# Kernel tuning notes

Hardware: AMD Instinct MI355X
Metric: run time of the kernel (lower is better)

Reference implementation:

```python
import jax, jax.numpy as jnp
import numpy as np

N = 100000   # nodes
E = 1000000  # directed edges (before self-loops)
G = 512      # graphs in the batch
NEG_SLOPE = 0.2
EPS = 1e-5


def setup_inputs() -> dict:
    key = jax.random.key(0)
    ks = jax.random.split(key, 24)
    r = lambda i, shape, s=0.1: (jax.random.normal(ks[i], shape) * s).astype(jnp.float32)
    return {
        'x': jax.random.normal(ks[0], (N, 27), dtype=jnp.float32),
        'edge_index': jax.random.randint(ks[1], (2, E), 0, N, dtype=jnp.int32),
        'batch': jnp.sort(jax.random.randint(ks[2], (N,), 0, G, dtype=jnp.int32)),
        # GATv2Conv(26, 32, heads=2)
        'Wl1': r(3, (26, 64)), 'bl1': jnp.zeros(64, jnp.float32),
        'Wr1': r(4, (26, 64)), 'br1': jnp.zeros(64, jnp.float32),
        'att1': r(5, (2, 32)), 'b1': jnp.zeros(64, jnp.float32),
        'g1': jnp.ones(64, jnp.float32), 'be1': jnp.zeros(64, jnp.float32),
        # GATv2Conv(64, 32, heads=1)
        'Wl2': r(6, (64, 32)), 'bl2': jnp.zeros(32, jnp.float32),
        'Wr2': r(7, (64, 32)), 'br2': jnp.zeros(32, jnp.float32),
        'att2': r(8, (1, 32)), 'b2': jnp.zeros(32, jnp.float32),
        'g2': jnp.ones(32, jnp.float32), 'be2': jnp.zeros(32, jnp.float32),
        # gate_nn: 32 -> 16 -> 1
        'Wg1': r(9, (32, 16)), 'bg1': jnp.zeros(16, jnp.float32),
        'Wg2': r(10, (16, 1)), 'bg2': jnp.zeros(1, jnp.float32),
        # final head: 33 -> 16 -> 1
        'Wh1': r(11, (33, 16)), 'bh1': jnp.zeros(16, jnp.float32),
        'Wh2': r(12, (16, 1)), 'bh2': jnp.zeros(1, jnp.float32),
    }


def _gatv2(x, Wl, bl, Wr, br, att, bias, src, dst, heads, ch):
    n = x.shape[0]
    xl = (x @ Wl + bl).reshape(n, heads, ch)  # source projection (messages)
    xr = (x @ Wr + br).reshape(n, heads, ch)  # target projection
    e = jax.nn.leaky_relu(xl[src] + xr[dst], NEG_SLOPE)      # [Etot, H, C]
    logits = jnp.einsum('ehc,hc->eh', e, att)                 # [Etot, H]
    m = jax.ops.segment_max(logits, dst, num_segments=n)
    a = jnp.exp(logits - m[dst])
    z = jax.ops.segment_sum(a, dst, num_segments=n)
    a = a / (z[dst] + 1e-16)
    out = jax.ops.segment_sum(xl[src] * a[:, :, None], dst, num_segments=n)
    return out.reshape(n, heads * ch) + bias


def _batchnorm(h, gamma, beta):
    mu = h.mean(axis=0)
    var = jnp.var(h, axis=0)  # biased, matches torch normalization
    return (h - mu) * jax.lax.rsqrt(var + EPS) * gamma + beta


def reference(x, edge_index, batch, Wl1, bl1, Wr1, br1, att1, b1, g1, be1,
              Wl2, bl2, Wr2, br2, att2, b2, g2, be2,
              Wg1, bg1, Wg2, bg2, Wh1, bh1, Wh2, bh2):
    n = x.shape[0]
    loops = jnp.arange(n, dtype=edge_index.dtype)
    src = jnp.concatenate([edge_index[0], loops])
    dst = jnp.concatenate([edge_index[1], loops])
    x_no_cost = jnp.concatenate([x[:, :24], x[:, 25:]], axis=1)  # [N, 26]
    h = jax.nn.elu(_batchnorm(_gatv2(x_no_cost, Wl1, bl1, Wr1, br1, att1, b1, src, dst, 2, 32), g1, be1))
    # dropout is identity in eval mode
    h = jax.nn.elu(_batchnorm(_gatv2(h, Wl2, bl2, Wr2, br2, att2, b2, src, dst, 1, 32), g2, be2))
    # attentional aggregation: gate MLP + segment softmax over graphs
    gate = jax.nn.relu(h @ Wg1 + bg1) @ Wg2 + bg2               # [N, 1]
    gm = jax.ops.segment_max(gate, batch, num_segments=G)
    ga = jnp.exp(gate - gm[batch])
    gz = jax.ops.segment_sum(ga, batch, num_segments=G)
    ga = ga / (gz[batch] + 1e-16)
    h_pooled = jax.ops.segment_sum(ga * h, batch, num_segments=G)  # [G, 32]
    counts = jax.ops.segment_sum(jnp.ones((n, 1), x.dtype), batch, num_segments=G)
    root_costs = jax.ops.segment_sum(x[:, 24:25], batch, num_segments=G) / jnp.maximum(counts, 1.0)
    combined = jnp.concatenate([h_pooled, root_costs], axis=1)   # [G, 33]
    return jax.nn.relu(combined @ Wh1 + bh1) @ Wh2 + bh2         # [G, 1]
```

## Files before the change

### kernel.cpp

```cpp
#include <hip/hip_runtime.h>
#include <hip/hip_fp16.h>
#include <math.h>

#define NEG 0.2f
#define BN_EPS 1e-5f
#define BKT_W 256
#define CHUNK 4096


__global__ __launch_bounds__(256)
void hist_kernel(const int* __restrict__ ei, int E, int nbh, int nbkt, int* __restrict__ cnt)
{
    __shared__ int hist[512];
    for (int i = threadIdx.x; i < nbkt; i += 256) hist[i] = 0;
    __syncthreads();
    const int g0 = blockIdx.x * (CHUNK / 4);
    #pragma unroll
    for (int it = 0; it < CHUNK / 1024; ++it) {
        int e = (g0 + it * 256 + threadIdx.x) * 4;
        if (e + 3 < E) {
            int4 d4 = *(const int4*)(ei + E + e);
            atomicAdd(&hist[d4.x >> 8], 1);
            atomicAdd(&hist[d4.y >> 8], 1);
            atomicAdd(&hist[d4.z >> 8], 1);
            atomicAdd(&hist[d4.w >> 8], 1);
        } else {
            for (int k = 0; k < 4; ++k)
                if (e + k < E) atomicAdd(&hist[ei[E + e + k] >> 8], 1);
        }
    }
    __syncthreads();
    for (int i = threadIdx.x; i < nbkt; i += 256) cnt[(size_t)i * nbh + blockIdx.x] = hist[i];
}

__global__ __launch_bounds__(256)
void scan_block_kernel(const int* __restrict__ in, int* __restrict__ out,
                       int* __restrict__ bsum, int n)
{
    __shared__ int s[256];
    int i = blockIdx.x * 256 + threadIdx.x;
    int v = (i < n) ? in[i] : 0;
    s[threadIdx.x] = v;
    __syncthreads();
    for (int off = 1; off < 256; off <<= 1) {
        int t = (threadIdx.x >= off) ? s[threadIdx.x - off] : 0;
        __syncthreads();
        s[threadIdx.x] += t;
        __syncthreads();
    }
    if (i < n) out[i + 1] = s[threadIdx.x];
    if (threadIdx.x == 255) bsum[blockIdx.x] = s[255];
}

__global__ __launch_bounds__(512)
void scan_sums_kernel(int* __restrict__ bsum, int nb)
{
    __shared__ int s[512];
    int v = (threadIdx.x < nb) ? bsum[threadIdx.x] : 0;
    s[threadIdx.x] = v;
    __syncthreads();
    for (int off = 1; off < 512; off <<= 1) {
        int t = (threadIdx.x >= off) ? s[threadIdx.x - off] : 0;
        __syncthreads();
        s[threadIdx.x] += t;
        __syncthreads();
    }
    if (threadIdx.x < nb) bsum[threadIdx.x] = s[threadIdx.x] - v;
}

__global__ __launch_bounds__(256)
void scan_add_kernel(int* __restrict__ out, const int* __restrict__ bsum, int n)
{
    int i = blockIdx.x * 256 + threadIdx.x;
    if (i < n) out[i + 1] += bsum[blockIdx.x];
    if (i == 0) out[0] = 0;
}

__global__ __launch_bounds__(256)
void scat_kernel(const int* __restrict__ ei, int E, int nbh, int nbkt,
                 const int* __restrict__ base, int2* __restrict__ pairs)
{
    __shared__ int fill[512];
    __shared__ int lbase[512];
    for (int i = threadIdx.x; i < nbkt; i += 256) {
        fill[i]  = 0;
        lbase[i] = base[(size_t)i * nbh + blockIdx.x];
    }
    __syncthreads();
    const int g0 = blockIdx.x * (CHUNK / 4);
    #pragma unroll
    for (int it = 0; it < CHUNK / 1024; ++it) {
        int e = (g0 + it * 256 + threadIdx.x) * 4;
        if (e + 3 < E) {
            int4 s4 = *(const int4*)(ei + e);
            int4 d4 = *(const int4*)(ei + E + e);
            int b, r;
            b = d4.x >> 8; r = atomicAdd(&fill[b], 1); pairs[lbase[b] + r] = make_int2(s4.x, d4.x);
            b = d4.y >> 8; r = atomicAdd(&fill[b], 1); pairs[lbase[b] + r] = make_int2(s4.y, d4.y);
            b = d4.z >> 8; r = atomicAdd(&fill[b], 1); pairs[lbase[b] + r] = make_int2(s4.z, d4.z);
            b = d4.w >> 8; r = atomicAdd(&fill[b], 1); pairs[lbase[b] + r] = make_int2(s4.w, d4.w);
        } else {
            for (int k = 0; k < 4; ++k) {
                if (e + k < E) {
                    int s = ei[e + k], d = ei[E + e + k];
                    int b = d >> 8;
                    int r = atomicAdd(&fill[b], 1);
                    pairs[lbase[b] + r] = make_int2(s, d);
                }
            }
        }
    }
}

__global__ __launch_bounds__(256)
void bucket_build_kernel(const int2* __restrict__ pairs, const int* __restrict__ base,
                         int nbh, int nbkt, int n, int E,
                         int* __restrict__ rowptr, int* __restrict__ srcs,
                         int* __restrict__ perm)
{
    const int b     = blockIdx.x;
    const int start = base[(size_t)b * nbh];
    const int end   = base[(size_t)(b + 1) * nbh];
    __shared__ int hist[256], sc[256], dcnt[64], dbase[64];
    hist[threadIdx.x] = 0;
    if (threadIdx.x < 64) dcnt[threadIdx.x] = 0;
    __syncthreads();
    for (int j = start + threadIdx.x; j < end; j += 256)
        atomicAdd(&hist[pairs[j].y & 255], 1);
    __syncthreads();
    const int v = hist[threadIdx.x];
    sc[threadIdx.x] = v;
    __syncthreads();
    for (int off = 1; off < 256; off <<= 1) {
        int t = (threadIdx.x >= off) ? sc[threadIdx.x - off] : 0;
        __syncthreads();
        sc[threadIdx.x] += t;
        __syncthreads();
    }
    const int excl = sc[threadIdx.x] - v;
    const int d = b * 256 + threadIdx.x;
    int bin = 0, rnk = 0;
    if (d < n) {
        rowptr[d] = start + excl;
        bin = min(v, 63);
        rnk = atomicAdd(&dcnt[bin], 1);
    }
    if (b == nbkt - 1 && threadIdx.x == 0) rowptr[n] = E;
    __syncthreads();
    hist[threadIdx.x] = excl;
    __syncthreads();
    for (int j = start + threadIdx.x; j < end; j += 256) {
        int2 p = pairs[j];
        int r = atomicAdd(&hist[p.y & 255], 1);
        srcs[start + r] = p.x;
    }
    if (threadIdx.x < 64) dbase[threadIdx.x] = dcnt[threadIdx.x];
    __syncthreads();
    for (int off = 1; off < 64; off <<= 1) {
        int t = 0;
        if (threadIdx.x < 64 && threadIdx.x >= off) t = dbase[threadIdx.x - off];
        __syncthreads();
        if (threadIdx.x < 64) dbase[threadIdx.x] += t;
        __syncthreads();
    }
    if (d < n) perm[b * 256 + (dbase[bin] - dcnt[bin]) + rnk] = d;
}


__device__ __forceinline__ void gat_step4(const uint2 raw, const float* __restrict__ xrv,
                                          const float* __restrict__ at,
                                          float& z, float* __restrict__ acc)
{
    union { uint2 u; __half2 h[2]; } q; q.u = raw;
    const float2 a = __half22float2(q.h[0]);
    const float2 b = __half22float2(q.h[1]);
    float t, p = 0.f;
    t = a.x + xrv[0]; t = t > 0.f ? t : NEG * t; p += t * at[0];
    t = a.y + xrv[1]; t = t > 0.f ? t : NEG * t; p += t * at[1];
    t = b.x + xrv[2]; t = t > 0.f ? t : NEG * t; p += t * at[2];
    t = b.y + xrv[3]; t = t > 0.f ? t : NEG * t; p += t * at[3];
    p += __shfl_xor(p, 1, 64);
    p += __shfl_xor(p, 2, 64);
    p += __shfl_xor(p, 4, 64);
    const float w = __expf(p);
    z += w;
    acc[0] += w * a.x; acc[1] += w * a.y; acc[2] += w * b.x; acc[3] += w * b.y;
}

template<int HC>
__global__ __launch_bounds__(256)
void gat_fused_kernel(const __half* __restrict__ xl, const float* __restrict__ xr,
                      const float* __restrict__ att,
                      const int* __restrict__ rowptr, const int* __restrict__ srcs,
                      const int* __restrict__ perm,
                      float* __restrict__ outp, int n)
{
    constexpr int LPG = HC / 4;
    const int gid  = (blockIdx.x * 256 + threadIdx.x) / LPG;
    const int lane = threadIdx.x % LPG;
    if (gid >= n) return;
    const int d = perm[gid];

    float at[4], xrv[4];
    {
        const float4 a = *(const float4*)(att + lane * 4);
        at[0] = a.x; at[1] = a.y; at[2] = a.z; at[3] = a.w;
        const float4 x0 = *(const float4*)(xr + (size_t)d * HC + lane * 4);
        xrv[0] = x0.x; xrv[1] = x0.y; xrv[2] = x0.z; xrv[3] = x0.w;
    }

    float z = 0.f, acc[4] = {0.f, 0.f, 0.f, 0.f};
    gat_step4(*(const uint2*)(xl + (size_t)d * HC + lane * 4), xrv, at, z, acc);

    const int jb = rowptr[d], je = rowptr[d + 1];
    int j = jb;
    for (; j + 4 <= je; j += 4) {
        const int s0 = srcs[j], s1 = srcs[j + 1], s2 = srcs[j + 2], s3 = srcs[j + 3];
        const uint2 r0 = *(const uint2*)(xl + (size_t)s0 * HC + lane * 4);
        const uint2 r1 = *(const uint2*)(xl + (size_t)s1 * HC + lane * 4);
        const uint2 r2 = *(const uint2*)(xl + (size_t)s2 * HC + lane * 4);
        const uint2 r3 = *(const uint2*)(xl + (size_t)s3 * HC + lane * 4);
        gat_step4(r0, xrv, at, z, acc);
        gat_step4(r1, xrv, at, z, acc);
        gat_step4(r2, xrv, at, z, acc);
        gat_step4(r3, xrv, at, z, acc);
    }
    for (; j < je; ++j)
        gat_step4(*(const uint2*)(xl + (size_t)srcs[j] * HC + lane * 4), xrv, at, z, acc);

    const float inv = 1.f / (z + 1e-16f);
    *(float4*)(outp + (size_t)d * HC + lane * 4) =
        make_float4(acc[0] * inv, acc[1] * inv, acc[2] * inv, acc[3] * inv);
}

template<int K, int OC, bool DROP24, bool FUSE_NORM>
__global__ __launch_bounds__(256, 4)
void proj_kernel(const float* __restrict__ in, int in_stride,
                 const float* __restrict__ Wl, const float* __restrict__ bl,
                 const float* __restrict__ Wr, const float* __restrict__ br,
                 const float* __restrict__ stats, const float* __restrict__ gamma,
                 const float* __restrict__ beta, float inv_n,
                 __half* __restrict__ outl, float* __restrict__ outr, int n)
{
    constexpr int C2  = 2 * OC;
    constexpr int NCG = C2 / 4;
    constexpr int NRG = 256 / NCG;
    constexpr int TR  = NRG * 4;
    constexpr int XLD = (K + 3) & ~3;
    __shared__ float xs[TR][XLD];

    float na = 1.f, nb = 0.f;
    if constexpr (FUSE_NORM) {
        int kk  = threadIdx.x % K;
        float mu  = stats[kk] * inv_n;
        float var = stats[K + kk] * inv_n - mu * mu;
        float rs  = rsqrtf(var + BN_EPS) * gamma[kk];
        na = rs; nb = beta[kk] - mu * rs;
    }

    const int row0 = blockIdx.x * TR;
    for (int i = threadIdx.x; i < TR * K; i += 256) {
        int r = i / K, k = i - r * K;
        int row = row0 + r;
        float v = 0.f;
        if (row < n) {
            int sc = DROP24 ? (k < 24 ? k : k + 1) : k;
            v = in[(size_t)row * in_stride + sc];
            if constexpr (FUSE_NORM) {
                float t = v * na + nb;
                v = t > 0.f ? t : expm1f(t);
            }
        }
        xs[r][k] = v;
    }
    __syncthreads();

    const int cg = threadIdx.x % NCG;
    const int rg = threadIdx.x / NCG;
    const int c4 = cg * 4;
    const bool left = (c4 < OC);
    const float* __restrict__ Wp = left ? Wl : Wr;
    const int cc = left ? c4 : c4 - OC;
    const float4 b4 = *(const float4*)((left ? bl : br) + cc);

    float acc[4][4];
    #pragma unroll
    for (int ri = 0; ri < 4; ++ri) {
        acc[ri][0] = b4.x; acc[ri][1] = b4.y; acc[ri][2] = b4.z; acc[ri][3] = b4.w;
    }

    #pragma unroll 1
    for (int kb = 0; kb < K / 4; ++kb) {
        const float4 w0 = *(const float4*)(Wp + (size_t)(kb * 4 + 0) * OC + cc);
        const float4 w1 = *(const float4*)(Wp + (size_t)(kb * 4 + 1) * OC + cc);
        const float4 w2 = *(const float4*)(Wp + (size_t)(kb * 4 + 2) * OC + cc);
        const float4 w3 = *(const float4*)(Wp + (size_t)(kb * 4 + 3) * OC + cc);
        #pragma unroll
        for (int ri = 0; ri < 4; ++ri) {
            const float4 xv = *(const float4*)(&xs[rg * 4 + ri][kb * 4]);
            acc[ri][0] += xv.x * w0.x + xv.y * w1.x + xv.z * w2.x + xv.w * w3.x;
            acc[ri][1] += xv.x * w0.y + xv.y * w1.y + xv.z * w2.y + xv.w * w3.y;
            acc[ri][2] += xv.x * w0.z + xv.y * w1.z + xv.z * w2.z + xv.w * w3.z;
            acc[ri][3] += xv.x * w0.w + xv.y * w1.w + xv.z * w2.w + xv.w * w3.w;
        }
    }
    if constexpr ((K & 3) != 0) {
        #pragma unroll
        for (int k = K & ~3; k < K; ++k) {
            const float4 wk = *(const float4*)(Wp + (size_t)k * OC + cc);
            #pragma unroll
            for (int ri = 0; ri < 4; ++ri) {
                const float xk = xs[rg * 4 + ri][k];
                acc[ri][0] += xk * wk.x; acc[ri][1] += xk * wk.y;
                acc[ri][2] += xk * wk.z; acc[ri][3] += xk * wk.w;
            }
        }
    }

    #pragma unroll
    for (int ri = 0; ri < 4; ++ri) {
        const int row = row0 + rg * 4 + ri;
        if (row >= n) continue;
        if (left) {
            union { uint2 u; __half2 h[2]; } o;
            o.h[0] = __float22half2_rn(make_float2(acc[ri][0], acc[ri][1]));
            o.h[1] = __float22half2_rn(make_float2(acc[ri][2], acc[ri][3]));
            *(uint2*)(outl + (size_t)row * OC + cc) = o.u;
        } else {
            *(float4*)(outr + (size_t)row * OC + cc) =
                make_float4(acc[ri][0], acc[ri][1], acc[ri][2], acc[ri][3]);
        }
    }
}

template<int C>
__global__ __launch_bounds__(256)
void bn_stats_kernel(const float* __restrict__ h, int n, float* __restrict__ stats)
{
    constexpr int RPB = 256 / C;
    int col = threadIdx.x % C, rg = threadIdx.x / C;
    float s = 0.f, s2 = 0.f;
    for (int r = blockIdx.x * RPB + rg; r < n; r += gridDim.x * RPB) {
        float v = h[(size_t)r * C + col];
        s += v; s2 += v * v;
    }
    __shared__ float red0[256], red1[256];
    red0[threadIdx.x] = s; red1[threadIdx.x] = s2;
    __syncthreads();
    for (int st = 128; st >= C; st >>= 1) {
        if (threadIdx.x < st) {
            red0[threadIdx.x] += red0[threadIdx.x + st];
            red1[threadIdx.x] += red1[threadIdx.x + st];
        }
        __syncthreads();
    }
    if (threadIdx.x < C) {
        atomicAdd(&stats[threadIdx.x],     red0[threadIdx.x]);
        atomicAdd(&stats[C + threadIdx.x], red1[threadIdx.x]);
    }
}

__global__ __launch_bounds__(256)
void gate_norm_kernel(float* __restrict__ h2, int n,
                      const float* __restrict__ stats, const float* __restrict__ gamma,
                      const float* __restrict__ beta, float inv_n,
                      const float* __restrict__ Wg1, const float* __restrict__ bg1,
                      const float* __restrict__ Wg2, const float* __restrict__ bg2,
                      float* __restrict__ gate)
{
    __shared__ float W1[512], W2[16], B1[16], A_[32], B_[32];
    for (int i = threadIdx.x; i < 512; i += 256) W1[i] = Wg1[i];
    if (threadIdx.x < 16) { W2[threadIdx.x] = Wg2[threadIdx.x]; B1[threadIdx.x] = bg1[threadIdx.x]; }
    if (threadIdx.x < 32) {
        float mu  = stats[threadIdx.x] * inv_n;
        float var = stats[32 + threadIdx.x] * inv_n - mu * mu;
        float rs  = rsqrtf(var + BN_EPS) * gamma[threadIdx.x];
        A_[threadIdx.x] = rs;
        B_[threadIdx.x] = beta[threadIdx.x] - mu * rs;
    }
    __syncthreads();
    int node = blockIdx.x * 256 + threadIdx.x;
    if (node >= n) return;
    float* row = h2 + (size_t)node * 32;
    float v[32];
    #pragma unroll
    for (int j = 0; j < 8; ++j) {
        float4 r = *(const float4*)(row + j * 4);
        v[4*j] = r.x; v[4*j+1] = r.y; v[4*j+2] = r.z; v[4*j+3] = r.w;
    }
    #pragma unroll
    for (int k = 0; k < 32; ++k) {
        float t = v[k] * A_[k] + B_[k];
        v[k] = t > 0.f ? t : expm1f(t);
    }
    float hid[16];
    #pragma unroll
    for (int j = 0; j < 16; ++j) hid[j] = B1[j];
    #pragma unroll
    for (int k = 0; k < 32; ++k) {
        #pragma unroll
        for (int j = 0; j < 16; ++j) hid[j] += v[k] * W1[k * 16 + j];
    }
    float g = bg2[0];
    #pragma unroll
    for (int j = 0; j < 16; ++j) g += (hid[j] > 0.f ? hid[j] : 0.f) * W2[j];
    gate[node] = g;
    #pragma unroll
    for (int j = 0; j < 8; ++j)
        *(float4*)(row + j * 4) = make_float4(v[4*j], v[4*j+1], v[4*j+2], v[4*j+3]);
}

__global__ __launch_bounds__(256)
void pool_head_kernel(const float* __restrict__ h2, const float* __restrict__ gate,
                      const int* __restrict__ batch, const float* __restrict__ x,
                      int n, int xstride,
                      const float* __restrict__ Wh1, const float* __restrict__ bh1,
                      const float* __restrict__ Wh2, const float* __restrict__ bh2,
                      float* __restrict__ out)
{
    int g = blockIdx.x;
    __shared__ int sstart, send;
    if (threadIdx.x == 0) {
        int lo = 0, hi = n;
        while (lo < hi) { int mid = (lo + hi) >> 1; if (batch[mid] < g) lo = mid + 1; else hi = mid; }
        sstart = lo;
        hi = n;
        while (lo < hi) { int mid = (lo + hi) >> 1; if (batch[mid] < g + 1) lo = mid + 1; else hi = mid; }
        send = lo;
    }
    __syncthreads();
    const int start = sstart, end = send, cnt = end - start;

    __shared__ float red[256];
    float mx = -INFINITY;
    for (int i = start + threadIdx.x; i < end; i += 256) mx = fmaxf(mx, gate[i]);
    red[threadIdx.x] = mx; __syncthreads();
    for (int st = 128; st > 0; st >>= 1) {
        if (threadIdx.x < st) red[threadIdx.x] = fmaxf(red[threadIdx.x], red[threadIdx.x + st]);
        __syncthreads();
    }
    const float gm = red[0]; __syncthreads();

    float se = 0.f;
    for (int i = start + threadIdx.x; i < end; i += 256) se += expf(gate[i] - gm);
    red[threadIdx.x] = se; __syncthreads();
    for (int st = 128; st > 0; st >>= 1) {
        if (threadIdx.x < st) red[threadIdx.x] += red[threadIdx.x + st];
        __syncthreads();
    }
    const float gz = red[0]; __syncthreads();

    float rc = 0.f;
    for (int i = start + threadIdx.x; i < end; i += 256) rc += x[(size_t)i * xstride + 24];
    red[threadIdx.x] = rc; __syncthreads();
    for (int st = 128; st > 0; st >>= 1) {
        if (threadIdx.x < st) red[threadIdx.x] += red[threadIdx.x + st];
        __syncthreads();
    }
    const float root = red[0] / fmaxf((float)cnt, 1.f); __syncthreads();

    const int col = threadIdx.x % 32, rg = threadIdx.x / 32;
    float acc = 0.f;
    for (int i = start + rg; i < end; i += 8) acc += expf(gate[i] - gm) * h2[(size_t)i * 32 + col];
    red[threadIdx.x] = acc; __syncthreads();
    for (int st = 128; st >= 32; st >>= 1) {
        if (threadIdx.x < st) red[threadIdx.x] += red[threadIdx.x + st];
        __syncthreads();
    }
    __shared__ float comb[33];
    if (threadIdx.x < 32) comb[threadIdx.x] = red[threadIdx.x] / (gz + 1e-16f);
    if (threadIdx.x == 0) comb[32] = root;
    __syncthreads();

    __shared__ float hidr[16];
    if (threadIdx.x < 16) {
        float hv = bh1[threadIdx.x];
        #pragma unroll
        for (int k = 0; k < 33; ++k) hv += comb[k] * Wh1[k * 16 + threadIdx.x];
        hidr[threadIdx.x] = hv > 0.f ? hv : 0.f;
    }
    __syncthreads();
    if (threadIdx.x == 0) {
        float r = bh2[0];
        #pragma unroll
        for (int j = 0; j < 16; ++j) r += hidr[j] * Wh2[j];
        out[g] = r;
    }
}


extern "C" void kernel_launch(void* const* d_in, const int* in_sizes, int n_in,
                              void* d_out, int out_size, void* d_ws, size_t ws_size,
                              hipStream_t stream)
{
    const float* x    = (const float*)d_in[0];
    const int*   ei   = (const int*)d_in[1];
    const int*   batch= (const int*)d_in[2];
    const float* Wl1  = (const float*)d_in[3];
    const float* bl1  = (const float*)d_in[4];
    const float* Wr1  = (const float*)d_in[5];
    const float* br1  = (const float*)d_in[6];
    const float* att1 = (const float*)d_in[7];
    const float* g1   = (const float*)d_in[9];
    const float* be1  = (const float*)d_in[10];
    const float* Wl2  = (const float*)d_in[11];
    const float* bl2  = (const float*)d_in[12];
    const float* Wr2  = (const float*)d_in[13];
    const float* br2  = (const float*)d_in[14];
    const float* att2 = (const float*)d_in[15];
    const float* g2   = (const float*)d_in[17];
    const float* be2  = (const float*)d_in[18];
    const float* Wg1  = (const float*)d_in[19];
    const float* bg1  = (const float*)d_in[20];
    const float* Wg2  = (const float*)d_in[21];
    const float* bg2  = (const float*)d_in[22];
    const float* Wh1  = (const float*)d_in[23];
    const float* bh1  = (const float*)d_in[24];
    const float* Wh2  = (const float*)d_in[25];
    const float* bh2  = (const float*)d_in[26];

    const int n  = in_sizes[0] / 27;
    const int E  = in_sizes[1] / 2;
    const int G  = out_size;
    const float inv_n = 1.f / (float)n;

    const int nbkt = (n + BKT_W - 1) / BKT_W;
    const int nbh  = (E + CHUNK - 1) / CHUNK;
    const int SZ   = nbkt * nbh;
    const int NBs  = (SZ + 255) / 256;

    float* ws = (float*)d_ws;
    size_t off = 0;
    auto align4 = [&](size_t v) { return (v + 3) & ~(size_t)3; };
    float* st1 = ws + off; off += 128;
    float* st2 = ws + off; off += 64;
    const size_t zero_floats = off;
    int* cnt     = (int*)(ws + off); off = align4(off + SZ);
    int* basearr = (int*)(ws + off); off = align4(off + SZ + 1);
    int* bsum    = (int*)(ws + off); off = align4(off + 512);
    int* rowptr  = (int*)(ws + off); off = align4(off + n + 1);
    int* srcs    = (int*)(ws + off); off = align4(off + E);
    int* perm    = (int*)(ws + off); off = align4(off + n);
    __half* xl1h = (__half*)(ws + off); off += (size_t)n * 32;
    float* xr1   = ws + off; off += (size_t)n * 64;
    float* h1    = ws + off; off += (size_t)n * 64;
    float* h2    = ws + off; off += (size_t)n * 32;
    int2* pairs   = (int2*)h1;
    __half* xl2h  = xl1h;
    float* xr2    = xr1;
    float* gate   = xr1 + (size_t)n * 32;

    hipMemsetAsync(d_ws, 0, zero_floats * sizeof(float), stream);

    hist_kernel<<<nbh, 256, 0, stream>>>(ei, E, nbh, nbkt, cnt);
    scan_block_kernel<<<NBs, 256, 0, stream>>>(cnt, basearr, bsum, SZ);
    scan_sums_kernel<<<1, 512, 0, stream>>>(bsum, NBs);
    scan_add_kernel<<<NBs, 256, 0, stream>>>(basearr, bsum, SZ);
    scat_kernel<<<nbh, 256, 0, stream>>>(ei, E, nbh, nbkt, basearr, pairs);
    bucket_build_kernel<<<nbkt, 256, 0, stream>>>(pairs, basearr, nbh, nbkt, n, E, rowptr, srcs, perm);

    proj_kernel<26, 64, true, false><<<(n + 31) / 32, 256, 0, stream>>>(
        x, 27, Wl1, bl1, Wr1, br1, nullptr, nullptr, nullptr, 0.f, xl1h, xr1, n);
    gat_fused_kernel<64><<<(n * 16 + 255) / 256, 256, 0, stream>>>(
        xl1h, xr1, att1, rowptr, srcs, perm, h1, n);
    bn_stats_kernel<64><<<256, 256, 0, stream>>>(h1, n, st1);

    proj_kernel<64, 32, false, true><<<(n + 63) / 64, 256, 0, stream>>>(
        h1, 64, Wl2, bl2, Wr2, br2, st1, g1, be1, inv_n, xl2h, xr2, n);
    gat_fused_kernel<32><<<(n * 8 + 255) / 256, 256, 0, stream>>>(
        xl2h, xr2, att2, rowptr, srcs, perm, h2, n);
    bn_stats_kernel<32><<<256, 256, 0, stream>>>(h2, n, st2);

    gate_norm_kernel<<<(n + 255) / 256, 256, 0, stream>>>(
        h2, n, st2, g2, be2, inv_n, Wg1, bg1, Wg2, bg2, gate);
    pool_head_kernel<<<G, 256, 0, stream>>>(h2, gate, batch, x, n, 27, Wh1, bh1, Wh2, bh2, (float*)d_out);
}
```

Measured before the change: 263.0 us.

## Fuse layer-1 projection into histogram kernel and store intermediates in half

The layer-1 projection now runs as extra blocks of the edge histogram kernel, so both overlap in one launch. The target projections xr and the layer-1 GAT output h1 are stored in fp16 instead of fp32, which halves their memory traffic in the GAT, BN-stats and layer-2 projection kernels. The BN-stats grid is enlarged to 1024 blocks. The cost is lower precision for h1 and the xr values, plus a heterogeneous fused kernel.

```diff
diff --git a/kernel.cpp b/kernel.cpp
--- a/kernel.cpp
+++ b/kernel.cpp
@@ -8,29 +8,102 @@
 #define CHUNK 4096
 
 
-__global__ __launch_bounds__(256)
-void hist_kernel(const int* __restrict__ ei, int E, int nbh, int nbkt, int* __restrict__ cnt)
+__global__ __launch_bounds__(256, 4)
+void hist_proj1_kernel(const int* __restrict__ ei, int E, int nbh, int nbkt,
+                       int* __restrict__ cnt,
+                       const float* __restrict__ in, int in_stride,
+                       const float* __restrict__ Wl, const float* __restrict__ bl,
+                       const float* __restrict__ Wr, const float* __restrict__ br,
+                       __half* __restrict__ outl, __half* __restrict__ outr, int n)
 {
     __shared__ int hist[512];
-    for (int i = threadIdx.x; i < nbkt; i += 256) hist[i] = 0;
-    __syncthreads();
-    const int g0 = blockIdx.x * (CHUNK / 4);
-    #pragma unroll
-    for (int it = 0; it < CHUNK / 1024; ++it) {
-        int e = (g0 + it * 256 + threadIdx.x) * 4;
-        if (e + 3 < E) {
-            int4 d4 = *(const int4*)(ei + E + e);
-            atomicAdd(&hist[d4.x >> 8], 1);
-            atomicAdd(&hist[d4.y >> 8], 1);
-            atomicAdd(&hist[d4.z >> 8], 1);
-            atomicAdd(&hist[d4.w >> 8], 1);
-        } else {
-            for (int k = 0; k < 4; ++k)
-                if (e + k < E) atomicAdd(&hist[ei[E + e + k] >> 8], 1);
-        }
-    }
-    __syncthreads();
-    for (int i = threadIdx.x; i < nbkt; i += 256) cnt[(size_t)i * nbh + blockIdx.x] = hist[i];
+    __shared__ float xs[32][28];
+
+    if (blockIdx.x < nbh) {
+        const int bid = blockIdx.x;
+        for (int i = threadIdx.x; i < nbkt; i += 256) hist[i] = 0;
+        __syncthreads();
+        const int g0 = bid * (CHUNK / 4);
+        #pragma unroll
+        for (int it = 0; it < CHUNK / 1024; ++it) {
+            int e = (g0 + it * 256 + threadIdx.x) * 4;
+            if (e + 3 < E) {
+                int4 d4 = *(const int4*)(ei + E + e);
+                atomicAdd(&hist[d4.x >> 8], 1);
+                atomicAdd(&hist[d4.y >> 8], 1);
+                atomicAdd(&hist[d4.z >> 8], 1);
+                atomicAdd(&hist[d4.w >> 8], 1);
+            } else {
+                for (int k = 0; k < 4; ++k)
+                    if (e + k < E) atomicAdd(&hist[ei[E + e + k] >> 8], 1);
+            }
+        }
+        __syncthreads();
+        for (int i = threadIdx.x; i < nbkt; i += 256) cnt[(size_t)i * nbh + bid] = hist[i];
+    } else {
+        constexpr int K = 26, OC = 64, NCG = 32;
+        const int row0 = (blockIdx.x - nbh) * 32;
+        for (int i = threadIdx.x; i < 32 * K; i += 256) {
+            int r = i / K, k = i - r * K;
+            int row = row0 + r;
+            float v = 0.f;
+            if (row < n) {
+                int sc = (k < 24) ? k : k + 1;
+                v = in[(size_t)row * in_stride + sc];
+            }
+            xs[r][k] = v;
+        }
+        __syncthreads();
+
+        const int cg = threadIdx.x % NCG;
+        const int rg = threadIdx.x / NCG;
+        const int c4 = cg * 4;
+        const bool left = (c4 < OC);
+        const float* __restrict__ Wp = left ? Wl : Wr;
+        const int cc = left ? c4 : c4 - OC;
+        const float4 b4 = *(const float4*)((left ? bl : br) + cc);
+
+        float acc[4][4];
+        #pragma unroll
+        for (int ri = 0; ri < 4; ++ri) {
+            acc[ri][0] = b4.x; acc[ri][1] = b4.y; acc[ri][2] = b4.z; acc[ri][3] = b4.w;
+        }
+        #pragma unroll 1
+        for (int kb = 0; kb < K / 4; ++kb) {
+            const float4 w0 = *(const float4*)(Wp + (size_t)(kb * 4 + 0) * OC + cc);
+            const float4 w1 = *(const float4*)(Wp + (size_t)(kb * 4 + 1) * OC + cc);
+            const float4 w2 = *(const float4*)(Wp + (size_t)(kb * 4 + 2) * OC + cc);
+            const float4 w3 = *(const float4*)(Wp + (size_t)(kb * 4 + 3) * OC + cc);
+            #pragma unroll
+            for (int ri = 0; ri < 4; ++ri) {
+                const float4 xv = *(const float4*)(&xs[rg * 4 + ri][kb * 4]);
+                acc[ri][0] += xv.x * w0.x + xv.y * w1.x + xv.z * w2.x + xv.w * w3.x;
+                acc[ri][1] += xv.x * w0.y + xv.y * w1.y + xv.z * w2.y + xv.w * w3.y;
+                acc[ri][2] += xv.x * w0.z + xv.y * w1.z + xv.z * w2.z + xv.w * w3.z;
+                acc[ri][3] += xv.x * w0.w + xv.y * w1.w + xv.z * w2.w + xv.w * w3.w;
+            }
+        }
+        #pragma unroll
+        for (int k = 24; k < K; ++k) {
+            const float4 wk = *(const float4*)(Wp + (size_t)k * OC + cc);
+            #pragma unroll
+            for (int ri = 0; ri < 4; ++ri) {
+                const float xk = xs[rg * 4 + ri][k];
+                acc[ri][0] += xk * wk.x; acc[ri][1] += xk * wk.y;
+                acc[ri][2] += xk * wk.z; acc[ri][3] += xk * wk.w;
+            }
+        }
+        __half* __restrict__ outp = left ? outl : outr;
+        #pragma unroll
+        for (int ri = 0; ri < 4; ++ri) {
+            const int row = row0 + rg * 4 + ri;
+            if (row >= n) continue;
+            union { uint2 u; __half2 h[2]; } o;
+            o.h[0] = __float22half2_rn(make_float2(acc[ri][0], acc[ri][1]));
+            o.h[1] = __float22half2_rn(make_float2(acc[ri][2], acc[ri][3]));
+            *(uint2*)(outp + (size_t)row * OC + cc) = o.u;
+        }
+    }
 }
 
 __global__ __launch_bounds__(256)
@@ -187,13 +260,13 @@
     acc[0] += w * a.x; acc[1] += w * a.y; acc[2] += w * b.x; acc[3] += w * b.y;
 }
 
-template<int HC>
-__global__ __launch_bounds__(256)
-void gat_fused_kernel(const __half* __restrict__ xl, const float* __restrict__ xr,
+template<int HC, bool OUT_HALF>
+__global__ __launch_bounds__(256)
+void gat_fused_kernel(const __half* __restrict__ xl, const __half* __restrict__ xr,
                       const float* __restrict__ att,
                       const int* __restrict__ rowptr, const int* __restrict__ srcs,
                       const int* __restrict__ perm,
-                      float* __restrict__ outp, int n)
+                      void* __restrict__ outp, int n)
 {
     constexpr int LPG = HC / 4;
     const int gid  = (blockIdx.x * 256 + threadIdx.x) / LPG;
@@ -205,8 +278,11 @@
     {
         const float4 a = *(const float4*)(att + lane * 4);
         at[0] = a.x; at[1] = a.y; at[2] = a.z; at[3] = a.w;
-        const float4 x0 = *(const float4*)(xr + (size_t)d * HC + lane * 4);
-        xrv[0] = x0.x; xrv[1] = x0.y; xrv[2] = x0.z; xrv[3] = x0.w;
+        union { uint2 u; __half2 h[2]; } qx;
+        qx.u = *(const uint2*)(xr + (size_t)d * HC + lane * 4);
+        const float2 x0 = __half22float2(qx.h[0]);
+        const float2 x1 = __half22float2(qx.h[1]);
+        xrv[0] = x0.x; xrv[1] = x0.y; xrv[2] = x1.x; xrv[3] = x1.y;
     }
 
     float z = 0.f, acc[4] = {0.f, 0.f, 0.f, 0.f};
@@ -229,34 +305,37 @@
         gat_step4(*(const uint2*)(xl + (size_t)srcs[j] * HC + lane * 4), xrv, at, z, acc);
 
     const float inv = 1.f / (z + 1e-16f);
-    *(float4*)(outp + (size_t)d * HC + lane * 4) =
-        make_float4(acc[0] * inv, acc[1] * inv, acc[2] * inv, acc[3] * inv);
-}
-
-template<int K, int OC, bool DROP24, bool FUSE_NORM>
+    if constexpr (OUT_HALF) {
+        union { uint2 u; __half2 h[2]; } o;
+        o.h[0] = __float22half2_rn(make_float2(acc[0] * inv, acc[1] * inv));
+        o.h[1] = __float22half2_rn(make_float2(acc[2] * inv, acc[3] * inv));
+        *(uint2*)((__half*)outp + (size_t)d * HC + lane * 4) = o.u;
+    } else {
+        *(float4*)((float*)outp + (size_t)d * HC + lane * 4) =
+            make_float4(acc[0] * inv, acc[1] * inv, acc[2] * inv, acc[3] * inv);
+    }
+}
+
+template<int K, int OC>
 __global__ __launch_bounds__(256, 4)
-void proj_kernel(const float* __restrict__ in, int in_stride,
-                 const float* __restrict__ Wl, const float* __restrict__ bl,
-                 const float* __restrict__ Wr, const float* __restrict__ br,
-                 const float* __restrict__ stats, const float* __restrict__ gamma,
-                 const float* __restrict__ beta, float inv_n,
-                 __half* __restrict__ outl, float* __restrict__ outr, int n)
+void proj2_kernel(const __half* __restrict__ in,
+                  const float* __restrict__ Wl, const float* __restrict__ bl,
+                  const float* __restrict__ Wr, const float* __restrict__ br,
+                  const float* __restrict__ stats, const float* __restrict__ gamma,
+                  const float* __restrict__ beta, float inv_n,
+                  __half* __restrict__ outl, __half* __restrict__ outr, int n)
 {
     constexpr int C2  = 2 * OC;
     constexpr int NCG = C2 / 4;
     constexpr int NRG = 256 / NCG;
     constexpr int TR  = NRG * 4;
-    constexpr int XLD = (K + 3) & ~3;
-    __shared__ float xs[TR][XLD];
-
-    float na = 1.f, nb = 0.f;
-    if constexpr (FUSE_NORM) {
-        int kk  = threadIdx.x % K;
-        float mu  = stats[kk] * inv_n;
-        float var = stats[K + kk] * inv_n - mu * mu;
-        float rs  = rsqrtf(var + BN_EPS) * gamma[kk];
-        na = rs; nb = beta[kk] - mu * rs;
-    }
+    __shared__ float xs[TR][K];
+
+    const int kk  = threadIdx.x % K;
+    const float mu  = stats[kk] * inv_n;
+    const float var = stats[K + kk] * inv_n - mu * mu;
+    const float rs  = rsqrtf(var + BN_EPS) * gamma[kk];
+    const float na = rs, nb = beta[kk] - mu * rs;
 
     const int row0 = blockIdx.x * TR;
     for (int i = threadIdx.x; i < TR * K; i += 256) {
@@ -264,12 +343,8 @@
         int row = row0 + r;
         float v = 0.f;
         if (row < n) {
-            int sc = DROP24 ? (k < 24 ? k : k + 1) : k;
-            v = in[(size_t)row * in_stride + sc];
-            if constexpr (FUSE_NORM) {
-                float t = v * na + nb;
-                v = t > 0.f ? t : expm1f(t);
-            }
+            float t = __half2float(in[(size_t)row * K + k]) * na + nb;
+            v = t > 0.f ? t : expm1f(t);
         }
         xs[r][k] = v;
     }
@@ -304,44 +379,30 @@
             acc[ri][3] += xv.x * w0.w + xv.y * w1.w + xv.z * w2.w + xv.w * w3.w;
         }
     }
-    if constexpr ((K & 3) != 0) {
-        #pragma unroll
-        for (int k = K & ~3; k < K; ++k) {
-            const float4 wk = *(const float4*)(Wp + (size_t)k * OC + cc);
-            #pragma unroll
-            for (int ri = 0; ri < 4; ++ri) {
-                const float xk = xs[rg * 4 + ri][k];
-                acc[ri][0] += xk * wk.x; acc[ri][1] += xk * wk.y;
-                acc[ri][2] += xk * wk.z; acc[ri][3] += xk * wk.w;
-            }
-        }
-    }
-
+
+    __half* __restrict__ outp = left ? outl : outr;
     #pragma unroll
     for (int ri = 0; ri < 4; ++ri) {
         const int row = row0 + rg * 4 + ri;
         if (row >= n) continue;
-        if (left) {
-            union { uint2 u; __half2 h[2]; } o;
-            o.h[0] = __float22half2_rn(make_float2(acc[ri][0], acc[ri][1]));
-            o.h[1] = __float22half2_rn(make_float2(acc[ri][2], acc[ri][3]));
-            *(uint2*)(outl + (size_t)row * OC + cc) = o.u;
-        } else {
-            *(float4*)(outr + (size_t)row * OC + cc) =
-                make_float4(acc[ri][0], acc[ri][1], acc[ri][2], acc[ri][3]);
-        }
-    }
-}
-
-template<int C>
-__global__ __launch_bounds__(256)
-void bn_stats_kernel(const float* __restrict__ h, int n, float* __restrict__ stats)
+        union { uint2 u; __half2 h[2]; } o;
+        o.h[0] = __float22half2_rn(make_float2(acc[ri][0], acc[ri][1]));
+        o.h[1] = __float22half2_rn(make_float2(acc[ri][2], acc[ri][3]));
+        *(uint2*)(outp + (size_t)row * OC + cc) = o.u;
+    }
+}
+
+template<int C, bool IN_HALF>
+__global__ __launch_bounds__(256)
+void bn_stats_kernel(const void* __restrict__ h, int n, float* __restrict__ stats)
 {
     constexpr int RPB = 256 / C;
     int col = threadIdx.x % C, rg = threadIdx.x / C;
     float s = 0.f, s2 = 0.f;
     for (int r = blockIdx.x * RPB + rg; r < n; r += gridDim.x * RPB) {
-        float v = h[(size_t)r * C + col];
+        float v;
+        if constexpr (IN_HALF) v = __half2float(((const __half*)h)[(size_t)r * C + col]);
+        else                   v = ((const float*)h)[(size_t)r * C + col];
         s += v; s2 += v * v;
     }
     __shared__ float red0[256], red1[256];
@@ -528,6 +589,7 @@
     const int nbh  = (E + CHUNK - 1) / CHUNK;
     const int SZ   = nbkt * nbh;
     const int NBs  = (SZ + 255) / 256;
+    const int npr1 = (n + 31) / 32;
 
     float* ws = (float*)d_ws;
     size_t off = 0;
@@ -542,34 +604,33 @@
     int* srcs    = (int*)(ws + off); off = align4(off + E);
     int* perm    = (int*)(ws + off); off = align4(off + n);
     __half* xl1h = (__half*)(ws + off); off += (size_t)n * 32;
-    float* xr1   = ws + off; off += (size_t)n * 64;
-    float* h1    = ws + off; off += (size_t)n * 64;
+    __half* xr1h = (__half*)(ws + off); off += (size_t)n * 32;
+    __half* h1h  = (__half*)(ws + off); off += (size_t)n * 32;
     float* h2    = ws + off; off += (size_t)n * 32;
-    int2* pairs   = (int2*)h1;
+    float* gate  = ws + off; off += (size_t)n;
+    int2* pairs   = (int2*)h1h;
     __half* xl2h  = xl1h;
-    float* xr2    = xr1;
-    float* gate   = xr1 + (size_t)n * 32;
+    __half* xr2h  = xr1h;
 
     hipMemsetAsync(d_ws, 0, zero_floats * sizeof(float), stream);
 
-    hist_kernel<<<nbh, 256, 0, stream>>>(ei, E, nbh, nbkt, cnt);
+    hist_proj1_kernel<<<nbh + npr1, 256, 0, stream>>>(
+        ei, E, nbh, nbkt, cnt, x, 27, Wl1, bl1, Wr1, br1, xl1h, xr1h, n);
     scan_block_kernel<<<NBs, 256, 0, stream>>>(cnt, basearr, bsum, SZ);
     scan_sums_kernel<<<1, 512, 0, stream>>>(bsum, NBs);
     scan_add_kernel<<<NBs, 256, 0, stream>>>(basearr, bsum, SZ);
     scat_kernel<<<nbh, 256, 0, stream>>>(ei, E, nbh, nbkt, basearr, pairs);
     bucket_build_kernel<<<nbkt, 256, 0, stream>>>(pairs, basearr, nbh, nbkt, n, E, rowptr, srcs, perm);
 
-    proj_kernel<26, 64, true, false><<<(n + 31) / 32, 256, 0, stream>>>(
-        x, 27, Wl1, bl1, Wr1, br1, nullptr, nullptr, nullptr, 0.f, xl1h, xr1, n);
-    gat_fused_kernel<64><<<(n * 16 + 255) / 256, 256, 0, stream>>>(
-        xl1h, xr1, att1, rowptr, srcs, perm, h1, n);
-    bn_stats_kernel<64><<<256, 256, 0, stream>>>(h1, n, st1);
-
-    proj_kernel<64, 32, false, true><<<(n + 63) / 64, 256, 0, stream>>>(
-        h1, 64, Wl2, bl2, Wr2, br2, st1, g1, be1, inv_n, xl2h, xr2, n);
-    gat_fused_kernel<32><<<(n * 8 + 255) / 256, 256, 0, stream>>>(
-        xl2h, xr2, att2, rowptr, srcs, perm, h2, n);
-    bn_stats_kernel<32><<<256, 256, 0, stream>>>(h2, n, st2);
+    gat_fused_kernel<64, true><<<(n * 16 + 255) / 256, 256, 0, stream>>>(
+        xl1h, xr1h, att1, rowptr, srcs, perm, h1h, n);
+    bn_stats_kernel<64, true><<<1024, 256, 0, stream>>>(h1h, n, st1);
+
+    proj2_kernel<64, 32><<<(n + 63) / 64, 256, 0, stream>>>(
+        h1h, Wl2, bl2, Wr2, br2, st1, g1, be1, inv_n, xl2h, xr2h, n);
+    gat_fused_kernel<32, false><<<(n * 8 + 255) / 256, 256, 0, stream>>>(
+        xl2h, xr2h, att2, rowptr, srcs, perm, h2, n);
+    bn_stats_kernel<32, false><<<1024, 256, 0, stream>>>(h2, n, st2);
 
     gate_norm_kernel<<<(n + 255) / 256, 256, 0, stream>>>(
         h2, n, st2, g2, be2, inv_n, Wg1, bg1, Wg2, bg2, gate);
```

Result: no change. 264.6 us (+0.6%).
